# Optimization experiments

Measured on AMD Instinct MI355X. Metric: run time of the kernel, lower is better.

The kernel has to match this reference:

```python
import jax, jax.numpy as jnp
import numpy as np

# ---- constant kernels (kornia canny defaults) ----

def _gauss_kernel1d(ksize=5, sigma=1.0):
    x = np.arange(ksize, dtype=np.float32) - (ksize - 1) / 2.0
    g = np.exp(-(x ** 2) / (2.0 * sigma ** 2))
    return (g / g.sum()).astype(np.float32)

_GK = _gauss_kernel1d()
_SOBEL_X = np.array([[-1, 0, 1], [-2, 0, 2], [-1, 0, 1]], np.float32) / 8.0  # normalized=True
_SOBEL_Y = _SOBEL_X.T.copy()

# 8 directional NMS kernels: +1 at center, -1 at neighbor d*45 degrees (kornia order)
_NMS = np.zeros((8, 1, 3, 3), np.float32)
_OFFS = [(0, 1), (1, 1), (1, 0), (1, -1), (0, -1), (-1, -1), (-1, 0), (-1, 1)]
for _i, (_dy, _dx) in enumerate(_OFFS):
    _NMS[_i, 0, 1, 1] = 1.0
    _NMS[_i, 0, 1 + _dy, 1 + _dx] = -1.0


def _conv(x, k):
    return jax.lax.conv_general_dilated(
        x, k, (1, 1), 'VALID', dimension_numbers=('NCHW', 'OIHW', 'NCHW'))


def _canny_dilate(x):
    # x: [B,3,H,W] BGR in [0,1]
    x = x[:, ::-1]  # bgr -> rgb
    gray = 0.299 * x[:, 0:1] + 0.587 * x[:, 1:2] + 0.114 * x[:, 2:3]  # [B,1,H,W]

    # gaussian blur 5x5, sigma=1, reflect padding (separable)
    p = jnp.pad(gray, ((0, 0), (0, 0), (2, 2), (2, 2)), mode='reflect')
    kh = jnp.asarray(_GK).reshape(1, 1, 1, 5)
    kv = jnp.asarray(_GK).reshape(1, 1, 5, 1)
    blurred = _conv(_conv(p, kh), kv)

    # sobel gradients, replicate padding
    sp = jnp.pad(blurred, ((0, 0), (0, 0), (1, 1), (1, 1)), mode='edge')
    sob = jnp.asarray(np.stack([_SOBEL_X, _SOBEL_Y])[:, None])  # (2,1,3,3)
    g = _conv(sp, sob)
    gx, gy = g[:, 0:1], g[:, 1:2]

    mag = jnp.sqrt(gx * gx + gy * gy + 1e-6)  # [B,1,H,W]
    ang45 = jnp.round(jnp.arctan2(gy, gx) * (180.0 / np.pi) / 45.0)  # multiples of 45 deg
    pos_idx = jnp.mod(ang45, 8).astype(jnp.int32)
    neg_idx = jnp.mod(ang45 + 4, 8).astype(jnp.int32)

    # direction-dependent non-maximum suppression
    nms = _conv(jnp.pad(mag, ((0, 0), (0, 0), (1, 1), (1, 1))), jnp.asarray(_NMS))  # [B,8,H,W]
    pos = jnp.take_along_axis(nms, pos_idx, axis=1)
    neg = jnp.take_along_axis(nms, neg_idx, axis=1)
    is_max = jnp.minimum(pos, neg) > 0.0
    mag = mag * is_max

    # morphological dilation, 5x5 ones kernel, geodesic border (pad with -max_val)
    MAX_VAL = 1e4
    padded = jnp.pad(mag, ((0, 0), (0, 0), (2, 2), (2, 2)), constant_values=-MAX_VAL)
    out = jax.lax.reduce_window(padded, -jnp.inf, jax.lax.max,
                                (1, 1, 5, 5), (1, 1, 1, 1), 'VALID')
    return out


def setup_inputs() -> dict:
    key = jax.random.key(0)
    x = jax.random.uniform(key, (32, 3, 512, 512), dtype=jnp.float32)
    return {'x': x}


def reference(x):
    return _canny_dilate(x)
```

## Files before the change

### kernel.cpp

```cpp
#include <hip/hip_runtime.h>
#include <math.h>

#define TILE 32
#define GSZ  44
#define BSZ  40
#define MSZ  38
#define KSZ  36

#define OFF_GRAY 0
#define OFF_HB   7744
#define OFF_BLUR 14784
#define OFF_MAG  21184
#define OFF_IDX  26960
#define OFF_MSK  0
#define OFF_COL  7744
#define SMEM_BYTES 28416

__device__ __forceinline__ int reflect512(int i) {
    int a = i < 0 ? -i : i;
    int b = 1022 - a;
    return a < b ? a : b;
}

__global__ __launch_bounds__(256)
void canny_fused(const float* __restrict__ x, float* __restrict__ out) {
    __shared__ __align__(16) unsigned char smem[SMEM_BYTES];
    float (*s_gray)[GSZ]       = (float(*)[GSZ])(smem + OFF_GRAY);
    float (*s_hb)[BSZ]         = (float(*)[BSZ])(smem + OFF_HB);
    float (*s_blur)[BSZ]       = (float(*)[BSZ])(smem + OFF_BLUR);
    float (*s_mag)[MSZ]        = (float(*)[MSZ])(smem + OFF_MAG);
    unsigned char (*s_idx)[MSZ]= (unsigned char(*)[MSZ])(smem + OFF_IDX);
    float (*s_msk)[KSZ]        = (float(*)[KSZ])(smem + OFF_MSK);
    float (*s_col)[TILE]       = (float(*)[TILE])(smem + OFF_COL);

    const int tid = threadIdx.x;
    const int n   = blockIdx.z;
    const int ty0 = blockIdx.y * TILE;
    const int tx0 = blockIdx.x * TILE;

    const float* x0 = x + (size_t)n * 3 * 512 * 512;

    for (int i = tid; i < GSZ * GSZ; i += 256) {
        int ly = i / GSZ, lx = i - ly * GSZ;
        int gy = reflect512(ty0 - 6 + ly);
        int gx = reflect512(tx0 - 6 + lx);
        size_t o = (size_t)gy * 512 + gx;
        s_gray[ly][lx] = 0.299f * x0[2 * 512 * 512 + o]
                       + 0.587f * x0[1 * 512 * 512 + o]
                       + 0.114f * x0[o];
    }
    __syncthreads();

    const float GKW0 = 0.054488684549643f;
    const float GKW1 = 0.244201342003233f;
    const float GKW2 = 0.402619946931554f;

    for (int i = tid; i < GSZ * BSZ; i += 256) {
        int ly = i / BSZ, lx = i - ly * BSZ;
        const float* r = &s_gray[ly][lx];
        s_hb[ly][lx] = GKW0 * r[0] + GKW1 * r[1] + GKW2 * r[2]
                     + GKW1 * r[3] + GKW0 * r[4];
    }
    __syncthreads();

    for (int i = tid; i < BSZ * BSZ; i += 256) {
        int ly = i / BSZ, lx = i - ly * BSZ;
        s_blur[ly][lx] = GKW0 * s_hb[ly][lx]     + GKW1 * s_hb[ly + 1][lx]
                       + GKW2 * s_hb[ly + 2][lx] + GKW1 * s_hb[ly + 3][lx]
                       + GKW0 * s_hb[ly + 4][lx];
    }
    __syncthreads();

    for (int i = tid; i < MSZ * MSZ; i += 256) {
        int ly = i / MSZ, lx = i - ly * MSZ;
        int gy = ty0 - 3 + ly, gx = tx0 - 3 + lx;
        float magv = 0.f;
        unsigned char axis = 0;
        if (gy >= 0 && gy < 512 && gx >= 0 && gx < 512) {
            int ym = max(gy - 1, 0)   - (ty0 - 4);
            int y0 = gy               - (ty0 - 4);
            int yp = min(gy + 1, 511) - (ty0 - 4);
            int xm = max(gx - 1, 0)   - (tx0 - 4);
            int xc = gx               - (tx0 - 4);
            int xp = min(gx + 1, 511) - (tx0 - 4);
            float b00 = s_blur[ym][xm], b01 = s_blur[ym][xc], b02 = s_blur[ym][xp];
            float b10 = s_blur[y0][xm],                       b12 = s_blur[y0][xp];
            float b20 = s_blur[yp][xm], b21 = s_blur[yp][xc], b22 = s_blur[yp][xp];
            float gxv = 0.125f * (b02 - b00) + 0.25f * (b12 - b10) + 0.125f * (b22 - b20);
            float gyv = 0.125f * (b20 - b00) + 0.25f * (b21 - b01) + 0.125f * (b22 - b02);
            magv = sqrtf(gxv * gxv + gyv * gyv + 1e-6f);
            float ax = fabsf(gxv), ay = fabsf(gyv);
            if (ay <= 0.41421356237309515f * ax)      axis = 0;
            else if (ay >= 2.4142135623730951f * ax)  axis = 2;
            else axis = ((gxv >= 0.f) == (gyv >= 0.f)) ? 1 : 3;
        }
        s_mag[ly][lx] = magv;
        s_idx[ly][lx] = axis;
    }
    __syncthreads();

    const int offy[4] = {0, 1, 1, 1};
    const int offx[4] = {1, 1, 0, -1};
    for (int i = tid; i < KSZ * KSZ; i += 256) {
        int ly = i / KSZ, lx = i - ly * KSZ;
        int gy = ty0 - 2 + ly, gx = tx0 - 2 + lx;
        float v = 0.f;
        if (gy >= 0 && gy < 512 && gx >= 0 && gx < 512) {
            int my = ly + 1, mx = lx + 1;
            float m = s_mag[my][mx];
            int d = s_idx[my][mx];
            int dy = offy[d], dx = offx[d];
            float mp = 0.f, mn = 0.f;
            if (gy + dy >= 0 && gy + dy < 512 && gx + dx >= 0 && gx + dx < 512)
                mp = s_mag[my + dy][mx + dx];
            if (gy - dy >= 0 && gy - dy < 512 && gx - dx >= 0 && gx - dx < 512)
                mn = s_mag[my - dy][mx - dx];
            v = (fminf(m - mp, m - mn) > 0.f) ? m : 0.f;
        }
        s_msk[ly][lx] = v;
    }
    __syncthreads();

    for (int i = tid; i < KSZ * TILE; i += 256) {
        int ly = i / TILE, lx = i - ly * TILE;
        const float* r = &s_msk[ly][lx];
        float m01 = fmaxf(r[0], r[1]);
        float m23 = fmaxf(r[2], r[3]);
        s_col[ly][lx] = fmaxf(fmaxf(m01, m23), r[4]);
    }
    __syncthreads();

    for (int i = tid; i < TILE * TILE; i += 256) {
        int ly = i / TILE, lx = i - ly * TILE;
        float m01 = fmaxf(s_col[ly][lx],     s_col[ly + 1][lx]);
        float m23 = fmaxf(s_col[ly + 2][lx], s_col[ly + 3][lx]);
        float best = fmaxf(fmaxf(m01, m23), s_col[ly + 4][lx]);
        out[((size_t)n * 512 + ty0 + ly) * 512 + tx0 + lx] = best;
    }
}

extern "C" void kernel_launch(void* const* d_in, const int* in_sizes, int n_in,
                              void* d_out, int out_size, void* d_ws, size_t ws_size,
                              hipStream_t stream) {
    const float* x = (const float*)d_in[0];
    float* out = (float*)d_out;
    dim3 grid(512 / TILE, 512 / TILE, 32);
    canny_fused<<<grid, 256, 0, stream>>>(x, out);
}
```

Measured before the change: 213.6 us.

## Replace shared-memory tiled stages with per-wave vertical streaming pipeline using lane permutes

```diff
diff --git a/kernel.cpp b/kernel.cpp
--- a/kernel.cpp
+++ b/kernel.cpp
@@ -1,141 +1,117 @@
 #include <hip/hip_runtime.h>
 #include <math.h>
 
-#define TILE 32
-#define GSZ  44
-#define BSZ  40
-#define MSZ  38
-#define KSZ  36
-
-#define OFF_GRAY 0
-#define OFF_HB   7744
-#define OFF_BLUR 14784
-#define OFF_MAG  21184
-#define OFF_IDX  26960
-#define OFF_MSK  0
-#define OFF_COL  7744
-#define SMEM_BYTES 28416
+#define IMW 512
+#define SEG 32
+#define NSEG (512/SEG)
+#define NSTRIP 10
+#define OUTW 52
 
 __device__ __forceinline__ int reflect512(int i) {
     int a = i < 0 ? -i : i;
     int b = 1022 - a;
     return a < b ? a : b;
 }
+__device__ __forceinline__ float bperm(int a4, float v) {
+    return __int_as_float(__builtin_amdgcn_ds_bpermute(a4, __float_as_int(v)));
+}
 
 __global__ __launch_bounds__(256)
-void canny_fused(const float* __restrict__ x, float* __restrict__ out) {
-    __shared__ __align__(16) unsigned char smem[SMEM_BYTES];
-    float (*s_gray)[GSZ]       = (float(*)[GSZ])(smem + OFF_GRAY);
-    float (*s_hb)[BSZ]         = (float(*)[BSZ])(smem + OFF_HB);
-    float (*s_blur)[BSZ]       = (float(*)[BSZ])(smem + OFF_BLUR);
-    float (*s_mag)[MSZ]        = (float(*)[MSZ])(smem + OFF_MAG);
-    unsigned char (*s_idx)[MSZ]= (unsigned char(*)[MSZ])(smem + OFF_IDX);
-    float (*s_msk)[KSZ]        = (float(*)[KSZ])(smem + OFF_MSK);
-    float (*s_col)[TILE]       = (float(*)[TILE])(smem + OFF_COL);
+void canny_pipe(const float* __restrict__ x, float* __restrict__ out) {
+    const int lane  = threadIdx.x & 63;
+    const int unit  = blockIdx.x * 4 + (threadIdx.x >> 6);
+    const int img   = unit / (NSTRIP * NSEG);
+    const int rem   = unit - img * (NSTRIP * NSEG);
+    const int strip = rem / NSEG;
+    const int seg   = rem - strip * NSEG;
+    const int Y0 = seg * SEG, Y1 = Y0 + SEG;
+    const int x0 = strip * OUTW - 6;
+    const int xv = x0 + lane;
+    const int xr = reflect512(xv);
+    const bool inimg  = (xv >= 0) && (xv < IMW);
+    const bool stlane = (lane >= 6) && (lane < 58) && (xv < IMW);
+    const int l4  = lane << 2;
+    const int aL4 = (min(max(xv - 1, 0), 511) - x0) << 2;
+    const int aR4 = (min(max(xv + 1, 0), 511) - x0) << 2;
 
-    const int tid = threadIdx.x;
-    const int n   = blockIdx.z;
-    const int ty0 = blockIdx.y * TILE;
-    const int tx0 = blockIdx.x * TILE;
+    const float* base = x + (size_t)img * 3 * IMW * IMW;
+    const float* c0p = base + (size_t)0 * IMW * IMW + xr;
+    const float* c1p = base + (size_t)1 * IMW * IMW + xr;
+    const float* c2p = base + (size_t)2 * IMW * IMW + xr;
+    float* outp = out + (size_t)img * IMW * IMW + xv;
 
-    const float* x0 = x + (size_t)n * 3 * 512 * 512;
+    const float K0 = 0.054488684549643f, K1 = 0.244201342003233f, K2 = 0.402619946931554f;
 
-    for (int i = tid; i < GSZ * GSZ; i += 256) {
-        int ly = i / GSZ, lx = i - ly * GSZ;
-        int gy = reflect512(ty0 - 6 + ly);
-        int gx = reflect512(tx0 - 6 + lx);
-        size_t o = (size_t)gy * 512 + gx;
-        s_gray[ly][lx] = 0.299f * x0[2 * 512 * 512 + o]
-                       + 0.587f * x0[1 * 512 * 512 + o]
-                       + 0.114f * x0[o];
-    }
-    __syncthreads();
+    float hb0=0,hb1=0,hb2=0,hb3=0,hb4=0;
+    float hx0=0,hx1=0,hx2=0, hy0=0,hy1=0,hy2=0;
+    float mg0=0,mg1=0,mg2=0;
+    int   ax0=0, ax1=0;
+    float cm0=0,cm1=0,cm2=0,cm3=0,cm4=0;
 
-    const float GKW0 = 0.054488684549643f;
-    const float GKW1 = 0.244201342003233f;
-    const float GKW2 = 0.402619946931554f;
+    int r0 = reflect512(Y0 - 6);
+    float p0 = c0p[(size_t)r0 * IMW];
+    float p1 = c1p[(size_t)r0 * IMW];
+    float p2 = c2p[(size_t)r0 * IMW];
 
-    for (int i = tid; i < GSZ * BSZ; i += 256) {
-        int ly = i / BSZ, lx = i - ly * BSZ;
-        const float* r = &s_gray[ly][lx];
-        s_hb[ly][lx] = GKW0 * r[0] + GKW1 * r[1] + GKW2 * r[2]
-                     + GKW1 * r[3] + GKW0 * r[4];
-    }
-    __syncthreads();
+    for (int v = Y0 - 6; v <= Y1 + 5; ++v) {
+        float gray = 0.299f * p2 + 0.587f * p1 + 0.114f * p0;
+        int rn = reflect512(v + 1);
+        p0 = c0p[(size_t)rn * IMW];
+        p1 = c1p[(size_t)rn * IMW];
+        p2 = c2p[(size_t)rn * IMW];
 
-    for (int i = tid; i < BSZ * BSZ; i += 256) {
-        int ly = i / BSZ, lx = i - ly * BSZ;
-        s_blur[ly][lx] = GKW0 * s_hb[ly][lx]     + GKW1 * s_hb[ly + 1][lx]
-                       + GKW2 * s_hb[ly + 2][lx] + GKW1 * s_hb[ly + 3][lx]
-                       + GKW0 * s_hb[ly + 4][lx];
-    }
-    __syncthreads();
+        float gl1 = bperm(l4 - 4, gray), gl2 = bperm(l4 - 8, gray);
+        float gr1 = bperm(l4 + 4, gray), gr2 = bperm(l4 + 8, gray);
+        hb0 = hb1; hb1 = hb2; hb2 = hb3; hb3 = hb4;
+        hb4 = K0 * (gl2 + gr2) + K1 * (gl1 + gr1) + K2 * gray;
 
-    for (int i = tid; i < MSZ * MSZ; i += 256) {
-        int ly = i / MSZ, lx = i - ly * MSZ;
-        int gy = ty0 - 3 + ly, gx = tx0 - 3 + lx;
-        float magv = 0.f;
-        unsigned char axis = 0;
-        if (gy >= 0 && gy < 512 && gx >= 0 && gx < 512) {
-            int ym = max(gy - 1, 0)   - (ty0 - 4);
-            int y0 = gy               - (ty0 - 4);
-            int yp = min(gy + 1, 511) - (ty0 - 4);
-            int xm = max(gx - 1, 0)   - (tx0 - 4);
-            int xc = gx               - (tx0 - 4);
-            int xp = min(gx + 1, 511) - (tx0 - 4);
-            float b00 = s_blur[ym][xm], b01 = s_blur[ym][xc], b02 = s_blur[ym][xp];
-            float b10 = s_blur[y0][xm],                       b12 = s_blur[y0][xp];
-            float b20 = s_blur[yp][xm], b21 = s_blur[yp][xc], b22 = s_blur[yp][xp];
-            float gxv = 0.125f * (b02 - b00) + 0.25f * (b12 - b10) + 0.125f * (b22 - b20);
-            float gyv = 0.125f * (b20 - b00) + 0.25f * (b21 - b01) + 0.125f * (b22 - b02);
-            magv = sqrtf(gxv * gxv + gyv * gyv + 1e-6f);
-            float ax = fabsf(gxv), ay = fabsf(gyv);
-            if (ay <= 0.41421356237309515f * ax)      axis = 0;
-            else if (ay >= 2.4142135623730951f * ax)  axis = 2;
-            else axis = ((gxv >= 0.f) == (gyv >= 0.f)) ? 1 : 3;
+        float blur = K0 * (hb0 + hb4) + K1 * (hb1 + hb3) + K2 * hb2;
+        float bl = bperm(aL4, blur), br = bperm(aR4, blur);
+        hx0 = hx1; hx1 = hx2; hx2 = br - bl;
+        hy0 = hy1; hy1 = hy2; hy2 = bl + 2.f * blur + br;
+
+        int g = v - 3;
+        float hxa = (g == 0)   ? hx1 : hx0;
+        float hxc = (g == 511) ? hx1 : hx2;
+        float hya = (g == 0)   ? hy1 : hy0;
+        float hyc = (g == 511) ? hy1 : hy2;
+        float gxv = (hxa + 2.f * hx1 + hxc) * 0.125f;
+        float gyv = (hyc - hya) * 0.125f;
+        float mag = sqrtf(gxv * gxv + gyv * gyv + 1e-6f);
+        float axm = fabsf(gxv), aym = fabsf(gyv);
+        int axis;
+        if (aym <= 0.41421356237309515f * axm)      axis = 0;
+        else if (aym >= 2.4142135623730951f * axm)  axis = 2;
+        else axis = ((gxv >= 0.f) == (gyv >= 0.f)) ? 1 : 3;
+        mg0 = mg1; mg1 = mg2; mg2 = inimg ? mag : 0.f;
+        ax0 = ax1; ax1 = axis;
+
+        int m = v - 4;
+        float magm = (m == 0)   ? 0.f : mg0;
+        float magc = mg1;
+        float magp = (m == 511) ? 0.f : mg2;
+        float gcp = bperm(l4 + 4, magc), gcm = bperm(l4 - 4, magc);
+        float gpp = bperm(l4 + 4, magp), gpm = bperm(l4 - 4, magp);
+        float gmm = bperm(l4 - 4, magm), gmp = bperm(l4 + 4, magm);
+        int d = ax0;
+        float mp = (d == 0) ? gcp : (d == 1) ? gpp : (d == 2) ? magp : gpm;
+        float mn = (d == 0) ? gcm : (d == 1) ? gmm : (d == 2) ? magm : gmp;
+        float msk = (inimg && fminf(magc - mp, magc - mn) > 0.f) ? magc : 0.f;
+
+        float s1 = fmaxf(bperm(l4 - 4, msk), bperm(l4 + 4, msk));
+        float s2 = fmaxf(bperm(l4 - 8, msk), bperm(l4 + 8, msk));
+        cm0 = cm1; cm1 = cm2; cm2 = cm3; cm3 = cm4;
+        cm4 = fmaxf(fmaxf(s1, s2), msk);
+
+        int y = v - 6;
+        if (y >= Y0) {
+            float c0 = (y >= 2)   ? cm0 : 0.f;
+            float c1 = (y >= 1)   ? cm1 : 0.f;
+            float c3 = (y <= 510) ? cm3 : 0.f;
+            float c4 = (y <= 509) ? cm4 : 0.f;
+            float val = fmaxf(fmaxf(fmaxf(c0, c1), fmaxf(cm2, c3)), c4);
+            if (stlane) outp[(size_t)y * IMW] = val;
         }
-        s_mag[ly][lx] = magv;
-        s_idx[ly][lx] = axis;
-    }
-    __syncthreads();
-
-    const int offy[4] = {0, 1, 1, 1};
-    const int offx[4] = {1, 1, 0, -1};
-    for (int i = tid; i < KSZ * KSZ; i += 256) {
-        int ly = i / KSZ, lx = i - ly * KSZ;
-        int gy = ty0 - 2 + ly, gx = tx0 - 2 + lx;
-        float v = 0.f;
-        if (gy >= 0 && gy < 512 && gx >= 0 && gx < 512) {
-            int my = ly + 1, mx = lx + 1;
-            float m = s_mag[my][mx];
-            int d = s_idx[my][mx];
-            int dy = offy[d], dx = offx[d];
-            float mp = 0.f, mn = 0.f;
-            if (gy + dy >= 0 && gy + dy < 512 && gx + dx >= 0 && gx + dx < 512)
-                mp = s_mag[my + dy][mx + dx];
-            if (gy - dy >= 0 && gy - dy < 512 && gx - dx >= 0 && gx - dx < 512)
-                mn = s_mag[my - dy][mx - dx];
-            v = (fminf(m - mp, m - mn) > 0.f) ? m : 0.f;
-        }
-        s_msk[ly][lx] = v;
-    }
-    __syncthreads();
-
-    for (int i = tid; i < KSZ * TILE; i += 256) {
-        int ly = i / TILE, lx = i - ly * TILE;
-        const float* r = &s_msk[ly][lx];
-        float m01 = fmaxf(r[0], r[1]);
-        float m23 = fmaxf(r[2], r[3]);
-        s_col[ly][lx] = fmaxf(fmaxf(m01, m23), r[4]);
-    }
-    __syncthreads();
-
-    for (int i = tid; i < TILE * TILE; i += 256) {
-        int ly = i / TILE, lx = i - ly * TILE;
-        float m01 = fmaxf(s_col[ly][lx],     s_col[ly + 1][lx]);
-        float m23 = fmaxf(s_col[ly + 2][lx], s_col[ly + 3][lx]);
-        float best = fmaxf(fmaxf(m01, m23), s_col[ly + 4][lx]);
-        out[((size_t)n * 512 + ty0 + ly) * 512 + tx0 + lx] = best;
     }
 }
 
@@ -144,6 +120,7 @@
                               hipStream_t stream) {
     const float* x = (const float*)d_in[0];
     float* out = (float*)d_out;
-    dim3 grid(512 / TILE, 512 / TILE, 32);
-    canny_fused<<<grid, 256, 0, stream>>>(x, out);
+    const int units = 32 * NSTRIP * NSEG;
+    dim3 grid(units / 4);
+    canny_pipe<<<grid, 256, 0, stream>>>(x, out);
 }
```

Measured after the change: 175.1 us. 18.0% less time.
